# Optimization experiments

Hardware: AMD Instinct MI355X
Metric: run time of the kernel (lower is better)

Reference implementation:

```python
import jax, jax.numpy as jnp
import numpy as np

T, B, I, H = 2048, 256, 64, 256

def setup_inputs() -> dict:
    key = jax.random.key(0)
    ks = jax.random.split(key, 10)
    s_ih = 1.0 / np.sqrt(H)
    return {
        "input": jax.random.normal(ks[0], (T, B, I), dtype=jnp.float32),
        "hidden": jax.random.normal(ks[1], (1, B, 3), dtype=jnp.float32),
        # linear_dec: 3 -> H
        "W_dec": jax.random.normal(ks[2], (H, 3), dtype=jnp.float32) * (1.0 / np.sqrt(3.0)),
        "b_dec": jax.random.normal(ks[3], (H,), dtype=jnp.float32) * 0.01,
        # GRU weights (PyTorch layout: gates stacked r,z,n along first dim)
        "W_ih": jax.random.normal(ks[4], (3 * H, I), dtype=jnp.float32) * s_ih,
        "W_hh": jax.random.normal(ks[5], (3 * H, H), dtype=jnp.float32) * s_ih,
        "b_ih": jax.random.normal(ks[6], (3 * H,), dtype=jnp.float32) * s_ih,
        "b_hh": jax.random.normal(ks[7], (3 * H,), dtype=jnp.float32) * s_ih,
        # linear_out: H -> I
        "W_out": jax.random.normal(ks[8], (I, H), dtype=jnp.float32) * s_ih,
        "b_out": jax.random.normal(ks[9], (I,), dtype=jnp.float32) * 0.01,
    }

def reference(input, hidden, W_dec, b_dec, W_ih, W_hh, b_ih, b_hh, W_out, b_out):
    # use_linear: project 3-dim latent to hidden_size
    h = jnp.einsum('lbt,ht->lbh', hidden, W_dec)[0] + b_dec  # [B, H]
    # teacher forcing: step 0 uses zeroed first frame, steps 1..T-1 use input[0..T-2]
    xs = jnp.concatenate([jnp.zeros_like(input[:1]), input[:-1]], axis=0)  # [T, B, I]
    # precompute all input-side gate projections in one big GEMM
    gi = jnp.einsum('tbi,gi->tbg', xs, W_ih) + b_ih  # [T, B, 3H]
    def step(h, gi_t):
        gh = h @ W_hh.T + b_hh  # [B, 3H]
        i_r, i_z, i_n = jnp.split(gi_t, 3, axis=-1)
        h_r, h_z, h_n = jnp.split(gh, 3, axis=-1)
        r = jax.nn.sigmoid(i_r + h_r)
        z = jax.nn.sigmoid(i_z + h_z)
        n = jnp.tanh(i_n + r * h_n)
        h_new = (1.0 - z) * n + z * h
        return h_new, h_new
    _, hs = jax.lax.scan(step, h, gi)  # hs: [T, B, H]
    out = jnp.einsum('tbh,oh->tbo', hs, W_out) + b_out  # [T, B, I]
    return out.transpose(1, 0, 2)  # [B, T, I]
```

## Files before the change

### kernel.cpp

```cpp
#include <hip/hip_runtime.h>
#include <cmath>

namespace {
constexpr int T_STEPS = 2048;
constexpr int B_SZ = 256;
constexpr int I_SZ = 64;
constexpr int H_SZ = 256;
constexpr int BC = 16;
constexpr int NB = B_SZ / BC;
constexpr int NW = 16;
constexpr int NTHR = NW * 64;

constexpr int WHH_US = NW * 8 * 3 * 64 * 8;
constexpr int WIH_US = NW * 2 * 3 * 64 * 8;
constexpr int WOUT_US = NW * 2 * 64 * 8;
}

typedef __attribute__((ext_vector_type(8))) short s16x8;
typedef __attribute__((ext_vector_type(4))) short s16x4;
typedef __attribute__((ext_vector_type(4))) float f32x4;

__device__ __forceinline__ unsigned short bfr(float x) {
  unsigned u = __builtin_bit_cast(unsigned, x);
  u += 0x7fffu + ((u >> 16) & 1u);
  return (unsigned short)(u >> 16);
}

__device__ __forceinline__ int sigma_k(int g, int j) {
  return ((j >> 2) << 4) + (g << 2) + (j & 3);
}

__global__ void pack_whh(const float* __restrict__ W, unsigned short* __restrict__ dst) {
  int id = blockIdx.x * blockDim.x + threadIdx.x;
  if (id >= WHH_US) return;
  int j = id & 7, l = (id >> 3) & 63, g = (id / 512) % 3, kt = (id / 1536) & 7, w = id / 12288;
  int m = g * 256 + w * 16 + (l & 15);
  int k = kt * 32 + sigma_k(l >> 4, j);
  dst[id] = bfr(W[m * 256 + k]);
}
__global__ void pack_wih(const float* __restrict__ W, unsigned short* __restrict__ dst) {
  int id = blockIdx.x * blockDim.x + threadIdx.x;
  if (id >= WIH_US) return;
  int j = id & 7, l = (id >> 3) & 63, g = (id / 512) % 3, kt = (id / 1536) & 1, w = id / 3072;
  int m = g * 256 + w * 16 + (l & 15);
  int k = kt * 32 + sigma_k(l >> 4, j);
  dst[id] = bfr(W[m * 64 + k]);
}
__global__ void pack_wout(const float* __restrict__ W, unsigned short* __restrict__ dst) {
  int id = blockIdx.x * blockDim.x + threadIdx.x;
  if (id >= WOUT_US) return;
  int j = id & 7, l = (id >> 3) & 63, kk = (id / 512) & 1, w = id / 1024;
  int mt = w & 3, q = w >> 2;
  int m = mt * 16 + (l & 15);
  int k = (2 * q + kk) * 32 + sigma_k(l >> 4, j);
  dst[id] = bfr(W[m * 256 + k]);
}

__device__ __forceinline__ f32x4 MF(s16x8 a, s16x8 b, f32x4 c) {
  return __builtin_amdgcn_mfma_f32_16x16x32_bf16(a, b, c, 0, 0, 0);
}

__global__ __launch_bounds__(NTHR) void gru_mfma(
    const float* __restrict__ input,
    const float* __restrict__ hidden,
    const float* __restrict__ W_dec,
    const float* __restrict__ b_dec,
    const float* __restrict__ b_ih,
    const float* __restrict__ b_hh,
    const float* __restrict__ b_out,
    const unsigned short* __restrict__ wsp,
    float* __restrict__ out)
{
  __shared__ unsigned short h_buf[2][16 * 256];
  __shared__ unsigned short x_buf[2][16 * 64];
  __shared__ float po[4 * 16 * 64];
  __shared__ float bias_s[1024];

  const int tid = threadIdx.x;
  const int w = tid >> 6;
  const int l = tid & 63;
  const int c = l & 15;
  const int grp = l >> 4;
  const int b0 = blockIdx.x * BC;

  const s16x8* whh_p = (const s16x8*)(wsp);
  const s16x8* wih_p = (const s16x8*)(wsp + WHH_US);
  const s16x8* wout_p = (const s16x8*)(wsp + WHH_US + WIH_US);

  if (tid < 512) bias_s[tid] = b_ih[tid] + b_hh[tid];
  else if (tid < 768) bias_s[tid] = b_ih[tid];
  else bias_s[tid] = b_hh[tid - 256];
  x_buf[0][tid] = 0;

  const float bout = b_out[tid & 63];

  float hprev[4];
  {
    const float hv0 = hidden[(b0 + c) * 3 + 0];
    const float hv1 = hidden[(b0 + c) * 3 + 1];
    const float hv2 = hidden[(b0 + c) * 3 + 2];
    const int j0 = w * 16 + grp * 4;
    const int sw = c << 2;
    unsigned short hp[4];
#pragma unroll
    for (int i = 0; i < 4; ++i) {
      const int j = j0 + i;
      hprev[i] = fmaf(W_dec[j * 3 + 0], hv0,
                  fmaf(W_dec[j * 3 + 1], hv1,
                   fmaf(W_dec[j * 3 + 2], hv2, b_dec[j])));
      hp[i] = bfr(hprev[i]);
    }
    *(s16x4*)&h_buf[0][c * 256 + (j0 ^ sw)] = *(s16x4*)hp;
  }
  __syncthreads();

  const int j0v = w * 16 + grp * 4;
  const f32x4 brz_r = *(const f32x4*)&bias_s[j0v];
  const f32x4 brz_z = *(const f32x4*)&bias_s[256 + j0v];
  const f32x4 bni4 = *(const f32x4*)&bias_s[512 + j0v];
  const f32x4 bnh4 = *(const f32x4*)&bias_s[768 + j0v];
  const int sw = c << 2;

  for (int t = 0; t < T_STEPS; ++t) {
    const int p = t & 1;
    const unsigned short* hb = h_buf[p];
    const unsigned short* xb = x_buf[p];
    unsigned short* hbn = h_buf[p ^ 1];
    unsigned short* xbn = x_buf[p ^ 1];

    f32x4 ar{0.f, 0.f, 0.f, 0.f}, az{0.f, 0.f, 0.f, 0.f};
    f32x4 ani{0.f, 0.f, 0.f, 0.f}, anh{0.f, 0.f, 0.f, 0.f};

#pragma unroll
    for (int kt = 0; kt < 2; ++kt) {
      const int k0 = kt * 32 + (grp << 2);
      s16x4 lo = *(const s16x4*)&xb[c * 64 + (k0 ^ sw)];
      s16x4 hi = *(const s16x4*)&xb[c * 64 + ((k0 + 16) ^ sw)];
      s16x8 xf = __builtin_shufflevector(lo, hi, 0, 1, 2, 3, 4, 5, 6, 7);
      const int fb = ((w * 2 + kt) * 3) * 64 + l;
      ar = MF(wih_p[fb], xf, ar);
      az = MF(wih_p[fb + 64], xf, az);
      ani = MF(wih_p[fb + 128], xf, ani);
    }
#pragma unroll 2
    for (int kt = 0; kt < 8; ++kt) {
      const int k0 = kt * 32 + (grp << 2);
      s16x4 lo = *(const s16x4*)&hb[c * 256 + (k0 ^ sw)];
      s16x4 hi = *(const s16x4*)&hb[c * 256 + ((k0 + 16) ^ sw)];
      s16x8 hf = __builtin_shufflevector(lo, hi, 0, 1, 2, 3, 4, 5, 6, 7);
      const int fb = ((w * 8 + kt) * 3) * 64 + l;
      ar = MF(whh_p[fb], hf, ar);
      az = MF(whh_p[fb + 64], hf, az);
      anh = MF(whh_p[fb + 128], hf, anh);
    }

    unsigned short hp[4];
#pragma unroll
    for (int i = 0; i < 4; ++i) {
      const float r = 1.f / (1.f + __expf(-(ar[i] + brz_r[i])));
      const float z = 1.f / (1.f + __expf(-(az[i] + brz_z[i])));
      const float nn = tanhf(ani[i] + bni4[i] + r * (anh[i] + bnh4[i]));
      const float h = fmaf(z, hprev[i] - nn, nn);
      hprev[i] = h;
      hp[i] = bfr(h);
    }
    *(s16x4*)&hbn[c * 256 + (j0v ^ sw)] = *(s16x4*)hp;
    {
      const int xc = tid >> 6, xi = tid & 63;
      const float xv = input[((size_t)t * B_SZ + b0 + xc) * I_SZ + xi];
      xbn[xc * 64 + (xi ^ (xc << 2))] = bfr(xv);
    }
    __syncthreads();

    {
      const int mt = w & 3, q = w >> 2;
      f32x4 ao{0.f, 0.f, 0.f, 0.f};
#pragma unroll
      for (int kk = 0; kk < 2; ++kk) {
        const int kt = q * 2 + kk;
        const int k0 = kt * 32 + (grp << 2);
        s16x4 lo = *(const s16x4*)&hbn[c * 256 + (k0 ^ sw)];
        s16x4 hi = *(const s16x4*)&hbn[c * 256 + ((k0 + 16) ^ sw)];
        s16x8 hf = __builtin_shufflevector(lo, hi, 0, 1, 2, 3, 4, 5, 6, 7);
        ao = MF(wout_p[(w * 2 + kk) * 64 + l], hf, ao);
      }
      const int o0 = mt * 16 + grp * 4;
      *(f32x4*)&po[q * 1024 + c * 64 + (o0 ^ ((c & 7) << 2))] = ao;
    }
    __syncthreads();

    {
      const int oc = tid >> 6, oo = tid & 63;
      float v = bout;
#pragma unroll
      for (int q2 = 0; q2 < 4; ++q2)
        v += po[q2 * 1024 + oc * 64 + (oo ^ ((oc & 7) << 2))];
      out[((size_t)(b0 + oc) * T_STEPS + t) * I_SZ + oo] = v;
    }
  }
}

extern "C" void kernel_launch(void* const* d_in, const int* in_sizes, int n_in,
                              void* d_out, int out_size, void* d_ws, size_t ws_size,
                              hipStream_t stream) {
  const float* input  = (const float*)d_in[0];
  const float* hidden = (const float*)d_in[1];
  const float* W_dec  = (const float*)d_in[2];
  const float* b_dec  = (const float*)d_in[3];
  const float* W_ih   = (const float*)d_in[4];
  const float* W_hh   = (const float*)d_in[5];
  const float* b_ih   = (const float*)d_in[6];
  const float* b_hh   = (const float*)d_in[7];
  const float* W_out  = (const float*)d_in[8];
  const float* b_out  = (const float*)d_in[9];
  float* out = (float*)d_out;

  unsigned short* wsp = (unsigned short*)d_ws;

  pack_whh<<<(WHH_US + 255) / 256, 256, 0, stream>>>(W_hh, wsp);
  pack_wih<<<(WIH_US + 255) / 256, 256, 0, stream>>>(W_ih, wsp + WHH_US);
  pack_wout<<<(WOUT_US + 255) / 256, 256, 0, stream>>>(W_out, wsp + WHH_US + WIH_US);

  gru_mfma<<<NB, NTHR, 0, stream>>>(input, hidden, W_dec, b_dec,
                                    b_ih, b_hh, b_out, wsp, out);
}
```

Before: 10.45 ms.

## Keep W_hh in registers, W_ih in LDS, and drop output partial-sum reduction

The work is remapped from 16 waves to 8, with each wave owning two 16-row gate tiles. Each wave keeps its W_hh fragments resident in registers, and W_ih is staged once into shared memory, so the recurrent loop no longer refetches weights from global memory every timestep. Biases are loaded as the accumulator initial values. The output projection now runs over the full K in 4 waves and writes straight to global memory, which removes the LDS partial-sum buffer and one barrier per step. The previous hidden state is now read back as bf16 from shared memory instead of kept in fp32 registers, which loosens accuracy. The large register footprint combined with launch_bounds(…,2) risks spilling.

New measurement: 9.189 ms. 12.1% less time.

```diff
diff --git a/kernel.cpp b/kernel.cpp
--- a/kernel.cpp
+++ b/kernel.cpp
@@ -8,23 +8,27 @@
 constexpr int H_SZ = 256;
 constexpr int BC = 16;
 constexpr int NB = B_SZ / BC;
-constexpr int NW = 16;
+constexpr int NW = 8;
 constexpr int NTHR = NW * 64;
 
-constexpr int WHH_US = NW * 8 * 3 * 64 * 8;
-constexpr int WIH_US = NW * 2 * 3 * 64 * 8;
-constexpr int WOUT_US = NW * 2 * 64 * 8;
+constexpr int WHH_US = 16 * 3 * 8 * 64 * 8;
+constexpr int WIH_US = 16 * 3 * 2 * 64 * 8;
+constexpr int WOUT_US = 4 * 8 * 64 * 8;
 }
 
 typedef __attribute__((ext_vector_type(8))) short s16x8;
 typedef __attribute__((ext_vector_type(4))) short s16x4;
 typedef __attribute__((ext_vector_type(4))) float f32x4;
+typedef __attribute__((ext_vector_type(4))) unsigned int u32x4;
 
 __device__ __forceinline__ unsigned short bfr(float x) {
   unsigned u = __builtin_bit_cast(unsigned, x);
   u += 0x7fffu + ((u >> 16) & 1u);
   return (unsigned short)(u >> 16);
 }
+__device__ __forceinline__ float bf2f(unsigned short us) {
+  return __builtin_bit_cast(float, (unsigned)us << 16);
+}
 
 __device__ __forceinline__ int sigma_k(int g, int j) {
   return ((j >> 2) << 4) + (g << 2) + (j & 3);
@@ -33,26 +37,33 @@
 __global__ void pack_whh(const float* __restrict__ W, unsigned short* __restrict__ dst) {
   int id = blockIdx.x * blockDim.x + threadIdx.x;
   if (id >= WHH_US) return;
-  int j = id & 7, l = (id >> 3) & 63, g = (id / 512) % 3, kt = (id / 1536) & 7, w = id / 12288;
-  int m = g * 256 + w * 16 + (l & 15);
+  int j = id & 7, l = (id >> 3) & 63;
+  int F = id >> 9;
+  int kt = F & 7, gg = F >> 3;
+  int g = gg % 3, ws = gg / 3;
+  int m = g * 256 + ws * 16 + (l & 15);
   int k = kt * 32 + sigma_k(l >> 4, j);
   dst[id] = bfr(W[m * 256 + k]);
 }
 __global__ void pack_wih(const float* __restrict__ W, unsigned short* __restrict__ dst) {
   int id = blockIdx.x * blockDim.x + threadIdx.x;
   if (id >= WIH_US) return;
-  int j = id & 7, l = (id >> 3) & 63, g = (id / 512) % 3, kt = (id / 1536) & 1, w = id / 3072;
-  int m = g * 256 + w * 16 + (l & 15);
+  int j = id & 7, l = (id >> 3) & 63;
+  int f = id >> 9;
+  int kt = f & 1, gg = f >> 1;
+  int g = gg % 3, ws = gg / 3;
+  int m = g * 256 + ws * 16 + (l & 15);
   int k = kt * 32 + sigma_k(l >> 4, j);
   dst[id] = bfr(W[m * 64 + k]);
 }
 __global__ void pack_wout(const float* __restrict__ W, unsigned short* __restrict__ dst) {
   int id = blockIdx.x * blockDim.x + threadIdx.x;
   if (id >= WOUT_US) return;
-  int j = id & 7, l = (id >> 3) & 63, kk = (id / 512) & 1, w = id / 1024;
-  int mt = w & 3, q = w >> 2;
+  int j = id & 7, l = (id >> 3) & 63;
+  int f = id >> 9;
+  int kt = f & 7, mt = f >> 3;
   int m = mt * 16 + (l & 15);
-  int k = (2 * q + kk) * 32 + sigma_k(l >> 4, j);
+  int k = kt * 32 + sigma_k(l >> 4, j);
   dst[id] = bfr(W[m * 256 + k]);
 }
 
@@ -60,7 +71,7 @@
   return __builtin_amdgcn_mfma_f32_16x16x32_bf16(a, b, c, 0, 0, 0);
 }
 
-__global__ __launch_bounds__(NTHR) void gru_mfma(
+__global__ __launch_bounds__(NTHR, 2) void gru_mfma(
     const float* __restrict__ input,
     const float* __restrict__ hidden,
     const float* __restrict__ W_dec,
@@ -71,9 +82,9 @@
     const unsigned short* __restrict__ wsp,
     float* __restrict__ out)
 {
+  __shared__ unsigned short wih_s[WIH_US];
   __shared__ unsigned short h_buf[2][16 * 256];
   __shared__ unsigned short x_buf[2][16 * 64];
-  __shared__ float po[4 * 16 * 64];
   __shared__ float bias_s[1024];
 
   const int tid = threadIdx.x;
@@ -82,44 +93,54 @@
   const int c = l & 15;
   const int grp = l >> 4;
   const int b0 = blockIdx.x * BC;
+  const int sw = c << 2;
 
   const s16x8* whh_p = (const s16x8*)(wsp);
-  const s16x8* wih_p = (const s16x8*)(wsp + WHH_US);
   const s16x8* wout_p = (const s16x8*)(wsp + WHH_US + WIH_US);
 
-  if (tid < 512) bias_s[tid] = b_ih[tid] + b_hh[tid];
-  else if (tid < 768) bias_s[tid] = b_ih[tid];
-  else bias_s[tid] = b_hh[tid - 256];
-  x_buf[0][tid] = 0;
-
-  const float bout = b_out[tid & 63];
-
-  float hprev[4];
+  s16x8 whh[2][3][8];
+#pragma unroll
+  for (int s = 0; s < 2; ++s)
+#pragma unroll
+    for (int g = 0; g < 3; ++g)
+#pragma unroll
+      for (int kt = 0; kt < 8; ++kt)
+        whh[s][g][kt] = whh_p[((((w * 2 + s) * 3 + g) * 8) + kt) * 64 + l];
+
+  {
+    const u32x4* s4 = (const u32x4*)(wsp + WHH_US);
+    u32x4* d4 = (u32x4*)wih_s;
+#pragma unroll
+    for (int i = 0; i < WIH_US / 8 / NTHR; ++i)
+      d4[i * NTHR + tid] = s4[i * NTHR + tid];
+  }
+  bias_s[tid] = b_ih[tid] + b_hh[tid];
+  if (tid < 256) bias_s[512 + tid] = b_ih[512 + tid];
+  else bias_s[512 + tid] = b_hh[256 + tid];
+  *(unsigned*)&x_buf[0][tid * 2] = 0;
+
+  f32x4 bo4 = {0.f, 0.f, 0.f, 0.f};
+  if (w < 4) bo4 = *(const f32x4*)&b_out[w * 16 + grp * 4];
+
   {
     const float hv0 = hidden[(b0 + c) * 3 + 0];
     const float hv1 = hidden[(b0 + c) * 3 + 1];
     const float hv2 = hidden[(b0 + c) * 3 + 2];
-    const int j0 = w * 16 + grp * 4;
-    const int sw = c << 2;
-    unsigned short hp[4];
-#pragma unroll
-    for (int i = 0; i < 4; ++i) {
-      const int j = j0 + i;
-      hprev[i] = fmaf(W_dec[j * 3 + 0], hv0,
-                  fmaf(W_dec[j * 3 + 1], hv1,
-                   fmaf(W_dec[j * 3 + 2], hv2, b_dec[j])));
-      hp[i] = bfr(hprev[i]);
-    }
-    *(s16x4*)&h_buf[0][c * 256 + (j0 ^ sw)] = *(s16x4*)hp;
+#pragma unroll
+    for (int s = 0; s < 2; ++s) {
+      const int j0s = (w * 2 + s) * 16 + grp * 4;
+      unsigned short hp[4];
+#pragma unroll
+      for (int i = 0; i < 4; ++i) {
+        const int j = j0s + i;
+        hp[i] = bfr(fmaf(W_dec[j * 3 + 0], hv0,
+                     fmaf(W_dec[j * 3 + 1], hv1,
+                      fmaf(W_dec[j * 3 + 2], hv2, b_dec[j]))));
+      }
+      *(s16x4*)&h_buf[0][c * 256 + (j0s ^ sw)] = *(s16x4*)hp;
+    }
   }
   __syncthreads();
-
-  const int j0v = w * 16 + grp * 4;
-  const f32x4 brz_r = *(const f32x4*)&bias_s[j0v];
-  const f32x4 brz_z = *(const f32x4*)&bias_s[256 + j0v];
-  const f32x4 bni4 = *(const f32x4*)&bias_s[512 + j0v];
-  const f32x4 bnh4 = *(const f32x4*)&bias_s[768 + j0v];
-  const int sw = c << 2;
 
   for (int t = 0; t < T_STEPS; ++t) {
     const int p = t & 1;
@@ -128,8 +149,15 @@
     unsigned short* hbn = h_buf[p ^ 1];
     unsigned short* xbn = x_buf[p ^ 1];
 
-    f32x4 ar{0.f, 0.f, 0.f, 0.f}, az{0.f, 0.f, 0.f, 0.f};
-    f32x4 ani{0.f, 0.f, 0.f, 0.f}, anh{0.f, 0.f, 0.f, 0.f};
+    f32x4 ar[2], az[2], ani[2], anh[2];
+#pragma unroll
+    for (int s = 0; s < 2; ++s) {
+      const int m = (w * 2 + s) * 16 + grp * 4;
+      ar[s] = *(const f32x4*)&bias_s[m];
+      az[s] = *(const f32x4*)&bias_s[256 + m];
+      ani[s] = *(const f32x4*)&bias_s[512 + m];
+      anh[s] = *(const f32x4*)&bias_s[768 + m];
+    }
 
 #pragma unroll
     for (int kt = 0; kt < 2; ++kt) {
@@ -137,65 +165,65 @@
       s16x4 lo = *(const s16x4*)&xb[c * 64 + (k0 ^ sw)];
       s16x4 hi = *(const s16x4*)&xb[c * 64 + ((k0 + 16) ^ sw)];
       s16x8 xf = __builtin_shufflevector(lo, hi, 0, 1, 2, 3, 4, 5, 6, 7);
-      const int fb = ((w * 2 + kt) * 3) * 64 + l;
-      ar = MF(wih_p[fb], xf, ar);
-      az = MF(wih_p[fb + 64], xf, az);
-      ani = MF(wih_p[fb + 128], xf, ani);
-    }
-#pragma unroll 2
+#pragma unroll
+      for (int s = 0; s < 2; ++s) {
+        const int fb = (w * 2 + s) * 6 + kt;
+        ar[s]  = MF(*(const s16x8*)&wih_s[(fb    ) * 512 + l * 8], xf, ar[s]);
+        az[s]  = MF(*(const s16x8*)&wih_s[(fb + 2) * 512 + l * 8], xf, az[s]);
+        ani[s] = MF(*(const s16x8*)&wih_s[(fb + 4) * 512 + l * 8], xf, ani[s]);
+      }
+    }
+
+#pragma unroll
     for (int kt = 0; kt < 8; ++kt) {
       const int k0 = kt * 32 + (grp << 2);
       s16x4 lo = *(const s16x4*)&hb[c * 256 + (k0 ^ sw)];
       s16x4 hi = *(const s16x4*)&hb[c * 256 + ((k0 + 16) ^ sw)];
       s16x8 hf = __builtin_shufflevector(lo, hi, 0, 1, 2, 3, 4, 5, 6, 7);
-      const int fb = ((w * 8 + kt) * 3) * 64 + l;
-      ar = MF(whh_p[fb], hf, ar);
-      az = MF(whh_p[fb + 64], hf, az);
-      anh = MF(whh_p[fb + 128], hf, anh);
-    }
-
-    unsigned short hp[4];
-#pragma unroll
-    for (int i = 0; i < 4; ++i) {
-      const float r = 1.f / (1.f + __expf(-(ar[i] + brz_r[i])));
-      const float z = 1.f / (1.f + __expf(-(az[i] + brz_z[i])));
-      const float nn = tanhf(ani[i] + bni4[i] + r * (anh[i] + bnh4[i]));
-      const float h = fmaf(z, hprev[i] - nn, nn);
-      hprev[i] = h;
-      hp[i] = bfr(h);
-    }
-    *(s16x4*)&hbn[c * 256 + (j0v ^ sw)] = *(s16x4*)hp;
+#pragma unroll
+      for (int s = 0; s < 2; ++s) {
+        ar[s]  = MF(whh[s][0][kt], hf, ar[s]);
+        az[s]  = MF(whh[s][1][kt], hf, az[s]);
+        anh[s] = MF(whh[s][2][kt], hf, anh[s]);
+      }
+    }
+
+#pragma unroll
+    for (int s = 0; s < 2; ++s) {
+      const int j0s = (w * 2 + s) * 16 + grp * 4;
+      s16x4 hp4 = *(const s16x4*)&hb[c * 256 + (j0s ^ sw)];
+      unsigned short hpn[4];
+#pragma unroll
+      for (int i = 0; i < 4; ++i) {
+        const float r = 1.f / (1.f + __expf(-ar[s][i]));
+        const float z = 1.f / (1.f + __expf(-az[s][i]));
+        const float nn = tanhf(fmaf(r, anh[s][i], ani[s][i]));
+        const float h = fmaf(z, bf2f((unsigned short)hp4[i]) - nn, nn);
+        hpn[i] = bfr(h);
+      }
+      *(s16x4*)&hbn[c * 256 + (j0s ^ sw)] = *(s16x4*)hpn;
+    }
+
     {
-      const int xc = tid >> 6, xi = tid & 63;
-      const float xv = input[((size_t)t * B_SZ + b0 + xc) * I_SZ + xi];
-      xbn[xc * 64 + (xi ^ (xc << 2))] = bfr(xv);
+      const int xc = tid >> 5;
+      const int xi = (tid & 31) * 2;
+      const float* xs = &input[((size_t)t * B_SZ + b0 + xc) * I_SZ + xi];
+      const unsigned pk = (unsigned)bfr(xs[0]) | ((unsigned)bfr(xs[1]) << 16);
+      *(unsigned*)&xbn[xc * 64 + (xi ^ (xc << 2))] = pk;
     }
     __syncthreads();
 
-    {
-      const int mt = w & 3, q = w >> 2;
-      f32x4 ao{0.f, 0.f, 0.f, 0.f};
-#pragma unroll
-      for (int kk = 0; kk < 2; ++kk) {
-        const int kt = q * 2 + kk;
+    if (w < 4) {
+      f32x4 ao = bo4;
+#pragma unroll
+      for (int kt = 0; kt < 8; ++kt) {
         const int k0 = kt * 32 + (grp << 2);
         s16x4 lo = *(const s16x4*)&hbn[c * 256 + (k0 ^ sw)];
         s16x4 hi = *(const s16x4*)&hbn[c * 256 + ((k0 + 16) ^ sw)];
         s16x8 hf = __builtin_shufflevector(lo, hi, 0, 1, 2, 3, 4, 5, 6, 7);
-        ao = MF(wout_p[(w * 2 + kk) * 64 + l], hf, ao);
-      }
-      const int o0 = mt * 16 + grp * 4;
-      *(f32x4*)&po[q * 1024 + c * 64 + (o0 ^ ((c & 7) << 2))] = ao;
-    }
-    __syncthreads();
-
-    {
-      const int oc = tid >> 6, oo = tid & 63;
-      float v = bout;
-#pragma unroll
-      for (int q2 = 0; q2 < 4; ++q2)
-        v += po[q2 * 1024 + oc * 64 + (oo ^ ((oc & 7) << 2))];
-      out[((size_t)(b0 + oc) * T_STEPS + t) * I_SZ + oo] = v;
+        ao = MF(wout_p[(w * 8 + kt) * 64 + l], hf, ao);
+      }
+      *(f32x4*)&out[((size_t)(b0 + c) * T_STEPS + t) * I_SZ + w * 16 + grp * 4] = ao;
     }
   }
 }
```
